# Optimization experiments

Measured on AMD Instinct MI355X. Metric: run time of the kernel, lower is better.

The kernel has to match this reference:

```python
import jax, jax.numpy as jnp
import numpy as np

WS = (8, 8, 8)        # window size
SS = (4, 4, 4)        # shift size
HEADS = 4
DIM = 128
N = WS[0] * WS[1] * WS[2]  # 512 tokens per window


def _relative_position_index():
    # identical math to ShiftedWindowAttention.define_relative_position_index
    coords = np.stack(np.meshgrid(np.arange(WS[0]), np.arange(WS[1]), np.arange(WS[2]), indexing='ij'))
    cf = coords.reshape(3, -1)                       # [3, N]
    rel = (cf[:, :, None] - cf[:, None, :]).transpose(1, 2, 0).copy()  # [N, N, 3]
    rel[..., 0] += WS[0] - 1
    rel[..., 1] += WS[1] - 1
    rel[..., 2] += WS[2] - 1
    rel[..., 0] *= (2 * WS[2] - 1) * (2 * WS[1] - 1)
    rel[..., 1] *= 2 * WS[2] - 1
    return rel.sum(-1).reshape(-1).astype(np.int32)  # [N*N]


def _shift_attn_mask(H, W, D):
    # static shift mask, same as the torch slice-loop construction
    m = np.zeros((H, W, D), dtype=np.float32)
    hs = ((0, -WS[0]), (-WS[0], -SS[0]), (-SS[0], None))
    ws = ((0, -WS[1]), (-WS[1], -SS[1]), (-SS[1], None))
    ds = ((0, -WS[2]), (-WS[2], -SS[2]), (-SS[2], None))
    cnt = 0
    for h in hs:
        for w in ws:
            for d in ds:
                m[h[0]:h[1], w[0]:w[1], d[0]:d[1]] = cnt
                cnt += 1
    nH, nW, nD = H // WS[0], W // WS[1], D // WS[2]
    m = m.reshape(nH, WS[0], nW, WS[1], nD, WS[2]).transpose(0, 2, 4, 1, 3, 5).reshape(nH * nW * nD, N)
    diff = m[:, None, :] - m[:, :, None]
    return np.where(diff != 0, np.float32(-100.0), np.float32(0.0))  # [nWin, N, N]


def setup_inputs() -> dict:
    key = jax.random.key(0)
    ks = jax.random.split(key, 6)
    x = jax.random.normal(ks[0], (1, 32, 32, 32, DIM), dtype=jnp.float32)
    qkv_weight = jax.random.normal(ks[1], (3 * DIM, DIM), dtype=jnp.float32) * 0.02
    qkv_bias = jax.random.normal(ks[2], (3 * DIM,), dtype=jnp.float32) * 0.02
    proj_weight = jax.random.normal(ks[3], (DIM, DIM), dtype=jnp.float32) * 0.02
    proj_bias = jax.random.normal(ks[4], (DIM,), dtype=jnp.float32) * 0.02
    tbl = (2 * WS[0] - 1) * (2 * WS[1] - 1) * (2 * WS[2] - 1)
    rpb_table = jax.random.normal(ks[5], (tbl, HEADS), dtype=jnp.float32) * 0.02
    rp_index = jnp.asarray(_relative_position_index())
    return {"x": x, "qkv_weight": qkv_weight, "qkv_bias": qkv_bias,
            "proj_weight": proj_weight, "proj_bias": proj_bias,
            "rpb_table": rpb_table, "rp_index": rp_index}


def reference(x, qkv_weight, qkv_bias, proj_weight, proj_bias, rpb_table, rp_index):
    B, H, W, D, C = x.shape
    hd = C // HEADS
    # relative position bias: [1, heads, N, N]
    bias = rpb_table[rp_index].reshape(N, N, HEADS).transpose(2, 0, 1)[None]
    # cyclic shift (H,W,D divisible by window -> no padding branch)
    xs = jnp.roll(x, shift=(-SS[0], -SS[1], -SS[2]), axis=(1, 2, 3))
    nH, nW, nD = H // WS[0], W // WS[1], D // WS[2]
    nWin = nH * nW * nD
    # window partition -> [B*nWin, N, C]
    xw = xs.reshape(B, nH, WS[0], nW, WS[1], nD, WS[2], C)
    xw = xw.transpose(0, 1, 3, 5, 2, 4, 6, 7).reshape(B * nWin, N, C)
    qkv = xw @ qkv_weight.T + qkv_bias
    qkv = qkv.reshape(B * nWin, N, 3, HEADS, hd).transpose(2, 0, 3, 1, 4)
    q, k, v = qkv[0], qkv[1], qkv[2]          # each [B*nWin, heads, N, hd]
    q = q * jnp.float32(hd ** -0.5)
    attn = jnp.einsum('whnd,whmd->whnm', q, k) + bias
    mask = jnp.asarray(_shift_attn_mask(H, W, D))  # [nWin, N, N] static
    attn = attn.reshape(B, nWin, HEADS, N, N) + mask[None, :, None]
    attn = jax.nn.softmax(attn.reshape(B * nWin, HEADS, N, N), axis=-1)
    out = jnp.einsum('whnm,whmd->wnhd', attn, v).reshape(B * nWin, N, C)
    out = out @ proj_weight.T + proj_bias
    # reverse window partition
    out = out.reshape(B, nH, nW, nD, WS[0], WS[1], WS[2], C)
    out = out.transpose(0, 1, 4, 2, 5, 3, 6, 7).reshape(B, H, W, D, C)
    return jnp.roll(out, shift=(SS[0], SS[1], SS[2]), axis=(1, 2, 3))
```

## Files before the change

kernel.cpp:

```cpp
#include <hip/hip_runtime.h>
#include <hip/hip_bf16.h>
#include <math.h>


#define NTOT 262144

typedef float     f32x16 __attribute__((ext_vector_type(16)));
typedef __bf16    bf16x8 __attribute__((ext_vector_type(8)));
typedef _Float16  f16x8  __attribute__((ext_vector_type(8)));
typedef _Float16  f16x4  __attribute__((ext_vector_type(4)));
typedef unsigned int u32x4 __attribute__((ext_vector_type(4)));

__device__ __forceinline__ unsigned int pkbf16(float a, float b) {
  __hip_bfloat16 x = __float2bfloat16(a), y = __float2bfloat16(b);
  return (unsigned int)__builtin_bit_cast(unsigned short, x) |
         ((unsigned int)__builtin_bit_cast(unsigned short, y) << 16);
}
__device__ __forceinline__ unsigned short bfbits(float v) {
  return __builtin_bit_cast(unsigned short, __float2bfloat16(v));
}

__global__ void k_bias(const float* __restrict__ rpb, const int* __restrict__ rpi,
                       unsigned short* __restrict__ biasb,
                       const float* __restrict__ qkvw, const float* __restrict__ projw,
                       _Float16* __restrict__ wq, _Float16* __restrict__ wp) {
  int idx = blockIdx.x * 256 + threadIdx.x;
  int t = rpi[idx];
  float4 b4 = *reinterpret_cast<const float4*>(rpb + 4 * t);
  const float L2E = 1.4426950408889634f;
  biasb[0 * NTOT + idx] = bfbits(b4.x * L2E);
  biasb[1 * NTOT + idx] = bfbits(b4.y * L2E);
  biasb[2 * NTOT + idx] = bfbits(b4.z * L2E);
  biasb[3 * NTOT + idx] = bfbits(b4.w * L2E);
  if (idx < 65536) {
    if (idx < 49152) wq[idx] = (_Float16)qkvw[idx];
    else             wp[idx - 49152] = (_Float16)projw[idx - 49152];
  }
}

__global__ __launch_bounds__(256, 2) void k_qkv(
    const float* __restrict__ x, const _Float16* __restrict__ wq,
    const float* __restrict__ qkvb,
    __hip_bfloat16* __restrict__ qb, __hip_bfloat16* __restrict__ kb,
    __hip_bfloat16* __restrict__ vb) {
  __shared__ unsigned short As[128 * 128];
  __shared__ unsigned short Bs[128 * 128];
  const int tid = threadIdx.x;
  const int bm = blockIdx.x;
  const int nc = bm >> 8;
  const int mt = bm & 255;
  const int win = mt >> 2, t128 = mt & 3;
  const int wh = win >> 4, ww = (win >> 2) & 3, wd = win & 3;

#pragma unroll
  for (int u = 0; u < 8; ++u) {
    int f = u * 256 + tid;
    int row = f >> 4, seg = f & 15;
    int n = t128 * 128 + row;
    int lh = n >> 6, lw = (n >> 3) & 7, ld = n & 7;
    int sh = (wh * 8 + lh + 4) & 31;
    int sw = (ww * 8 + lw + 4) & 31;
    int sd = (wd * 8 + ld + 4) & 31;
    const float* src = x + ((sh * 32 + sw) * 32 + sd) * 128 + seg * 8;
    float4 a0 = *(const float4*)src;
    float4 a1 = *(const float4*)(src + 4);
    f16x8 hv;
    hv[0] = (_Float16)a0.x; hv[1] = (_Float16)a0.y;
    hv[2] = (_Float16)a0.z; hv[3] = (_Float16)a0.w;
    hv[4] = (_Float16)a1.x; hv[5] = (_Float16)a1.y;
    hv[6] = (_Float16)a1.z; hv[7] = (_Float16)a1.w;
    int slot = seg ^ (row & 15);
    *(u32x4*)(&As[row * 128 + slot * 8]) = __builtin_bit_cast(u32x4, hv);
  }
#pragma unroll
  for (int u = 0; u < 8; ++u) {
    int f = u * 256 + tid;
    int row = f >> 4, seg = f & 15;
    u32x4 wv = *(const u32x4*)(wq + (nc * 128 + row) * 128 + seg * 8);
    int slot = seg ^ (row & 15);
    *(u32x4*)(&Bs[row * 128 + slot * 8]) = wv;
  }
  __syncthreads();

  const int wave = tid >> 6, lane = tid & 63;
  const int lq = lane & 31, h = lane >> 5;
  const int wm = wave >> 1, wn = wave & 1;

  f32x16 a00, a01, a10, a11;
#pragma unroll
  for (int r = 0; r < 16; ++r) { a00[r] = 0.f; a01[r] = 0.f; a10[r] = 0.f; a11[r] = 0.f; }

#pragma unroll
  for (int ks = 0; ks < 8; ++ks) {
    int r0 = wm * 64 + lq, r1 = wm * 64 + 32 + lq;
    int c0 = wn * 64 + lq, c1 = wn * 64 + 32 + lq;
    int sl = ks * 2 + h;
    f16x8 af0 = __builtin_bit_cast(f16x8, *(const u32x4*)(&As[r0 * 128 + (sl ^ (r0 & 15)) * 8]));
    f16x8 af1 = __builtin_bit_cast(f16x8, *(const u32x4*)(&As[r1 * 128 + (sl ^ (r1 & 15)) * 8]));
    f16x8 bf0 = __builtin_bit_cast(f16x8, *(const u32x4*)(&Bs[c0 * 128 + (sl ^ (c0 & 15)) * 8]));
    f16x8 bf1 = __builtin_bit_cast(f16x8, *(const u32x4*)(&Bs[c1 * 128 + (sl ^ (c1 & 15)) * 8]));
    a00 = __builtin_amdgcn_mfma_f32_32x32x16_f16(af0, bf0, a00, 0, 0, 0);
    a01 = __builtin_amdgcn_mfma_f32_32x32x16_f16(af0, bf1, a01, 0, 0, 0);
    a10 = __builtin_amdgcn_mfma_f32_32x32x16_f16(af1, bf0, a10, 0, 0, 0);
    a11 = __builtin_amdgcn_mfma_f32_32x32x16_f16(af1, bf1, a11, 0, 0, 0);
  }

  const float scale = (float)(0.17677669529663687 * 1.4426950408889634);
  float bias0 = qkvb[nc * 128 + wn * 64 + lq];
  float bias1 = qkvb[nc * 128 + wn * 64 + 32 + lq];

#define EPI_QK(ACC, MI, NI, DST, DO_SCALE)                                    \
  {                                                                           \
    int head = wn * 2 + (NI);                                                 \
    size_t whb = (size_t)(win * 4 + head);                                    \
    float bc = (NI) ? bias1 : bias0;                                          \
    _Pragma("unroll")                                                         \
    for (int r = 0; r < 16; ++r) {                                            \
      int row32 = (r & 3) + 8 * (r >> 2) + 4 * h;                             \
      int n = t128 * 128 + wm * 64 + (MI) * 32 + row32;                       \
      float val = ACC[r] + bc;                                                \
      if (DO_SCALE) val *= scale;                                             \
      DST[(whb * 512 + n) * 32 + lq] = __float2bfloat16(val);                 \
    }                                                                         \
  }
#define EPI_V(ACC, MI, NI)                                                    \
  {                                                                           \
    int head = wn * 2 + (NI);                                                 \
    size_t whb = (size_t)(win * 4 + head);                                    \
    float bc = (NI) ? bias1 : bias0;                                          \
    _Pragma("unroll")                                                         \
    for (int g = 0; g < 4; ++g) {                                             \
      int n0 = t128 * 128 + wm * 64 + (MI) * 32 + g * 8 + 4 * h;              \
      uint2 u = make_uint2(pkbf16(ACC[g * 4 + 0] + bc, ACC[g * 4 + 1] + bc),  \
                           pkbf16(ACC[g * 4 + 2] + bc, ACC[g * 4 + 3] + bc)); \
      *(uint2*)(vb + (whb * 32 + lq) * 512 + n0) = u;                         \
    }                                                                         \
  }

  if (nc == 0) {
    EPI_QK(a00, 0, 0, qb, 1); EPI_QK(a01, 0, 1, qb, 1);
    EPI_QK(a10, 1, 0, qb, 1); EPI_QK(a11, 1, 1, qb, 1);
  } else if (nc == 1) {
    EPI_QK(a00, 0, 0, kb, 0); EPI_QK(a01, 0, 1, kb, 0);
    EPI_QK(a10, 1, 0, kb, 0); EPI_QK(a11, 1, 1, kb, 0);
  } else {
    EPI_V(a00, 0, 0); EPI_V(a01, 0, 1);
    EPI_V(a10, 1, 0); EPI_V(a11, 1, 1);
  }
}

__global__ __launch_bounds__(256) void k_attn(
    const __hip_bfloat16* __restrict__ qb, const __hip_bfloat16* __restrict__ kb,
    const __hip_bfloat16* __restrict__ vb, const unsigned short* __restrict__ biasb,
    _Float16* __restrict__ ao) {
  __shared__ unsigned short Ks[2][64 * 40];
  __shared__ unsigned short Vs[2][32 * 72];
  __shared__ unsigned char regid[512];

  const int tid = threadIdx.x;
  const int b = blockIdx.x;
  const int win = b >> 3, head = (b >> 1) & 3, half = b & 1;
  const int wh = win >> 4, ww = (win >> 2) & 3, wd = win & 3;
  const int wave = tid >> 6, lane = tid & 63;
  const int lq = lane & 31, h = lane >> 5;
  const int qA = half * 256 + wave * 64 + lq;
  const int qB = qA + 32;
  const bool has_mask = (wh == 3) || (ww == 3) || (wd == 3);

  unsigned rnA = 0, rnB = 0;
  if (has_mask) {
#pragma unroll
    for (int i = 0; i < 2; ++i) {
      int n = tid + i * 256;
      int lh = n >> 6, lw = (n >> 3) & 7, ld = n & 7;
      regid[n] = (unsigned char)(((wh == 3) ? (lh < 4 ? 1 : 2) : 0) * 9 +
                                 ((ww == 3) ? (lw < 4 ? 1 : 2) : 0) * 3 +
                                 ((wd == 3) ? (ld < 4 ? 1 : 2) : 0));
    }
    {
      int n = qA;
      int lh = n >> 6, lw = (n >> 3) & 7, ld = n & 7;
      rnA = (unsigned)(((wh == 3) ? (lh < 4 ? 1 : 2) : 0) * 9 +
                       ((ww == 3) ? (lw < 4 ? 1 : 2) : 0) * 3 +
                       ((wd == 3) ? (ld < 4 ? 1 : 2) : 0));
      n = qB; lh = n >> 6; lw = (n >> 3) & 7; ld = n & 7;
      rnB = (unsigned)(((wh == 3) ? (lh < 4 ? 1 : 2) : 0) * 9 +
                       ((ww == 3) ? (lw < 4 ? 1 : 2) : 0) * 3 +
                       ((wd == 3) ? (ld < 4 ? 1 : 2) : 0));
    }
  }

  const size_t whb = (size_t)(win * 4 + head);
  const __hip_bfloat16* qrowA = qb + (whb * 512 + qA) * 32;
  const __hip_bfloat16* qrowB = qb + (whb * 512 + qB) * 32;
  bf16x8 qfA0 = __builtin_bit_cast(bf16x8, *(const u32x4*)(qrowA + h * 8));
  bf16x8 qfA1 = __builtin_bit_cast(bf16x8, *(const u32x4*)(qrowA + 16 + h * 8));
  bf16x8 qfB0 = __builtin_bit_cast(bf16x8, *(const u32x4*)(qrowB + h * 8));
  bf16x8 qfB1 = __builtin_bit_cast(bf16x8, *(const u32x4*)(qrowB + 16 + h * 8));

  const __hip_bfloat16* kg = kb + whb * 512 * 32;
  const __hip_bfloat16* vg = vb + whb * 32 * 512;
  const unsigned short* browA = biasb + ((size_t)head * 512 + qA) * 512;
  const unsigned short* browB = biasb + ((size_t)head * 512 + qB) * 512;

  float lA = 0.f, lB = 0.f;
  f32x16 oA, oB;
#pragma unroll
  for (int r = 0; r < 16; ++r) { oA[r] = 0.f; oB[r] = 0.f; }

  const int srow = tid >> 2, sseg = tid & 3;
  const int svd = tid >> 3, sseg2 = tid & 7;
  u32x4 kreg, vreg;
#define GLOAD(CHK)                                                            \
  { kreg = *(const u32x4*)(kg + ((CHK) * 64 + srow) * 32 + sseg * 8);         \
    vreg = *(const u32x4*)(vg + svd * 512 + (CHK) * 64 + sseg2 * 8); }
#define LWRITE(BUF)                                                           \
  { *(u32x4*)(&Ks[BUF][srow * 40 + sseg * 8]) = kreg;                         \
    *(u32x4*)(&Vs[BUF][svd * 72 + sseg2 * 8]) = vreg; }

  GLOAD(0); LWRITE(0);
  __syncthreads();

  auto stream_step = [&](f32x16 c, const uint2* bb, unsigned rn,
                         float& l_run, f32x16& o,
                         bf16x8 vf0, bf16x8 vf1, int kbase) {
    float p[16];
#pragma unroll
    for (int j = 0; j < 4; ++j) {
      float b0 = __uint_as_float(bb[j].x << 16);
      float b1 = __uint_as_float(bb[j].x & 0xFFFF0000u);
      float b2 = __uint_as_float(bb[j].y << 16);
      float b3 = __uint_as_float(bb[j].y & 0xFFFF0000u);
      if (has_mask) {
        unsigned rm = *(const unsigned*)(&regid[kbase + h * 4 + j * 8]);
        b0 += ((rm & 255u) == rn) ? 0.f : -144.2695041f;
        b1 += (((rm >> 8) & 255u) == rn) ? 0.f : -144.2695041f;
        b2 += (((rm >> 16) & 255u) == rn) ? 0.f : -144.2695041f;
        b3 += (((rm >> 24)) == rn) ? 0.f : -144.2695041f;
      }
      p[j * 4 + 0] = exp2f(c[j * 4 + 0] + b0);
      p[j * 4 + 1] = exp2f(c[j * 4 + 1] + b1);
      p[j * 4 + 2] = exp2f(c[j * 4 + 2] + b2);
      p[j * 4 + 3] = exp2f(c[j * 4 + 3] + b3);
    }
    float s0 = (p[0] + p[1]) + (p[2] + p[3]);
    float s1 = (p[4] + p[5]) + (p[6] + p[7]);
    float s2 = (p[8] + p[9]) + (p[10] + p[11]);
    float s3 = (p[12] + p[13]) + (p[14] + p[15]);
    l_run += (s0 + s1) + (s2 + s3);
    unsigned bw[8];
#pragma unroll
    for (int g = 0; g < 8; ++g) bw[g] = pkbf16(p[2 * g], p[2 * g + 1]);
#pragma unroll
    for (int kc = 0; kc < 2; ++kc) {
      unsigned b0 = bw[kc * 4 + 0], b1 = bw[kc * 4 + 1];
      unsigned b2 = bw[kc * 4 + 2], b3 = bw[kc * 4 + 3];
      unsigned sb0 = __shfl_xor(b0, 32, 64), sb1 = __shfl_xor(b1, 32, 64);
      unsigned sb2 = __shfl_xor(b2, 32, 64), sb3 = __shfl_xor(b3, 32, 64);
      u32x4 pw;
      pw.x = h ? sb2 : b0;
      pw.y = h ? sb3 : b1;
      pw.z = h ? b2 : sb0;
      pw.w = h ? b3 : sb1;
      bf16x8 pf = __builtin_bit_cast(bf16x8, pw);
      o = __builtin_amdgcn_mfma_f32_32x32x16_bf16(kc ? vf1 : vf0, pf, o, 0, 0, 0);
    }
  };

  for (int chk = 0; chk < 8; ++chk) {
    const int cur = chk & 1;
    if (chk < 7) GLOAD(chk + 1);

#pragma unroll
    for (int sub = 0; sub < 2; ++sub) {
      const int kbase = chk * 64 + sub * 32;
      uint2 bbA[4], bbB[4];
#pragma unroll
      for (int j = 0; j < 4; ++j) {
        bbA[j] = *(const uint2*)(browA + kbase + h * 4 + j * 8);
        bbB[j] = *(const uint2*)(browB + kbase + h * 4 + j * 8);
      }
      const unsigned short* KsC = Ks[cur];
      const unsigned short* VsC = Vs[cur];
      bf16x8 kf0 = __builtin_bit_cast(bf16x8, *(const u32x4*)(&KsC[(sub * 32 + lq) * 40 + h * 8]));
      bf16x8 kf1 = __builtin_bit_cast(bf16x8, *(const u32x4*)(&KsC[(sub * 32 + lq) * 40 + 16 + h * 8]));
      f32x16 cA, cB;
#pragma unroll
      for (int r = 0; r < 16; ++r) { cA[r] = 0.f; cB[r] = 0.f; }
      cA = __builtin_amdgcn_mfma_f32_32x32x16_bf16(kf0, qfA0, cA, 0, 0, 0);
      cA = __builtin_amdgcn_mfma_f32_32x32x16_bf16(kf1, qfA1, cA, 0, 0, 0);
      cB = __builtin_amdgcn_mfma_f32_32x32x16_bf16(kf0, qfB0, cB, 0, 0, 0);
      cB = __builtin_amdgcn_mfma_f32_32x32x16_bf16(kf1, qfB1, cB, 0, 0, 0);
      bf16x8 vf0 = __builtin_bit_cast(bf16x8, *(const u32x4*)(&VsC[lq * 72 + sub * 32 + h * 8]));
      bf16x8 vf1 = __builtin_bit_cast(bf16x8, *(const u32x4*)(&VsC[lq * 72 + sub * 32 + 16 + h * 8]));
      stream_step(cA, bbA, rnA, lA, oA, vf0, vf1, kbase);
      stream_step(cB, bbB, rnB, lB, oB, vf0, vf1, kbase);
    }

    if (chk < 7) LWRITE(cur ^ 1);
    __syncthreads();
  }

  lA += __shfl_xor(lA, 32, 64);
  lB += __shfl_xor(lB, 32, 64);

  const float invA = 1.f / lA, invB = 1.f / lB;
  _Float16* orowA = ao + ((size_t)(win * 512 + qA)) * 128 + head * 32;
  _Float16* orowB = ao + ((size_t)(win * 512 + qB)) * 128 + head * 32;
#pragma unroll
  for (int j = 0; j < 4; ++j) {
    int d0 = j * 8 + h * 4;
    f16x4 tA, tB;
    tA[0] = (_Float16)(oA[j * 4 + 0] * invA); tA[1] = (_Float16)(oA[j * 4 + 1] * invA);
    tA[2] = (_Float16)(oA[j * 4 + 2] * invA); tA[3] = (_Float16)(oA[j * 4 + 3] * invA);
    tB[0] = (_Float16)(oB[j * 4 + 0] * invB); tB[1] = (_Float16)(oB[j * 4 + 1] * invB);
    tB[2] = (_Float16)(oB[j * 4 + 2] * invB); tB[3] = (_Float16)(oB[j * 4 + 3] * invB);
    *(f16x4*)(orowA + d0) = tA;
    *(f16x4*)(orowB + d0) = tB;
  }
}

__global__ __launch_bounds__(256, 2) void k_proj(
    const _Float16* __restrict__ ao, const _Float16* __restrict__ wp,
    const float* __restrict__ pb, float* __restrict__ out) {
  __shared__ unsigned short As[128 * 128];
  __shared__ unsigned short Bs[128 * 128];
  const int tid = threadIdx.x;
  const int mt = blockIdx.x;
  const int win = mt >> 2, t128 = mt & 3;
  const int wh = win >> 4, ww = (win >> 2) & 3, wd = win & 3;

#pragma unroll
  for (int u = 0; u < 8; ++u) {
    int f = u * 256 + tid;
    int row = f >> 4, seg = f & 15;
    u32x4 av = *(const u32x4*)(ao + ((size_t)(win * 512 + t128 * 128 + row)) * 128 + seg * 8);
    int slot = seg ^ (row & 15);
    *(u32x4*)(&As[row * 128 + slot * 8]) = av;
  }
#pragma unroll
  for (int u = 0; u < 8; ++u) {
    int f = u * 256 + tid;
    int row = f >> 4, seg = f & 15;
    u32x4 wv = *(const u32x4*)(wp + row * 128 + seg * 8);
    int slot = seg ^ (row & 15);
    *(u32x4*)(&Bs[row * 128 + slot * 8]) = wv;
  }
  __syncthreads();

  const int wave = tid >> 6, lane = tid & 63;
  const int lq = lane & 31, h = lane >> 5;
  const int wm = wave >> 1, wn = wave & 1;

  f32x16 a00, a01, a10, a11;
#pragma unroll
  for (int r = 0; r < 16; ++r) { a00[r] = 0.f; a01[r] = 0.f; a10[r] = 0.f; a11[r] = 0.f; }

#pragma unroll
  for (int ks = 0; ks < 8; ++ks) {
    int r0 = wm * 64 + lq, r1 = wm * 64 + 32 + lq;
    int c0 = wn * 64 + lq, c1 = wn * 64 + 32 + lq;
    int sl = ks * 2 + h;
    f16x8 af0 = __builtin_bit_cast(f16x8, *(const u32x4*)(&As[r0 * 128 + (sl ^ (r0 & 15)) * 8]));
    f16x8 af1 = __builtin_bit_cast(f16x8, *(const u32x4*)(&As[r1 * 128 + (sl ^ (r1 & 15)) * 8]));
    f16x8 bf0 = __builtin_bit_cast(f16x8, *(const u32x4*)(&Bs[c0 * 128 + (sl ^ (c0 & 15)) * 8]));
    f16x8 bf1 = __builtin_bit_cast(f16x8, *(const u32x4*)(&Bs[c1 * 128 + (sl ^ (c1 & 15)) * 8]));
    a00 = __builtin_amdgcn_mfma_f32_32x32x16_f16(af0, bf0, a00, 0, 0, 0);
    a01 = __builtin_amdgcn_mfma_f32_32x32x16_f16(af0, bf1, a01, 0, 0, 0);
    a10 = __builtin_amdgcn_mfma_f32_32x32x16_f16(af1, bf0, a10, 0, 0, 0);
    a11 = __builtin_amdgcn_mfma_f32_32x32x16_f16(af1, bf1, a11, 0, 0, 0);
  }

  float bias0 = pb[wn * 64 + lq];
  float bias1 = pb[wn * 64 + 32 + lq];

#define EPI_P(ACC, MI, NI)                                                    \
  {                                                                           \
    int col = wn * 64 + (NI) * 32 + lq;                                       \
    float bc = (NI) ? bias1 : bias0;                                          \
    _Pragma("unroll")                                                         \
    for (int r = 0; r < 16; ++r) {                                            \
      int row32 = (r & 3) + 8 * (r >> 2) + 4 * h;                             \
      int n = t128 * 128 + wm * 64 + (MI) * 32 + row32;                       \
      int lh = n >> 6, lw = (n >> 3) & 7, ld = n & 7;                         \
      int dh = (wh * 8 + lh + 4) & 31;                                        \
      int dw = (ww * 8 + lw + 4) & 31;                                        \
      int dd = (wd * 8 + ld + 4) & 31;                                        \
      out[(size_t)((dh * 32 + dw) * 32 + dd) * 128 + col] = ACC[r] + bc;      \
    }                                                                         \
  }
  EPI_P(a00, 0, 0); EPI_P(a01, 0, 1); EPI_P(a10, 1, 0); EPI_P(a11, 1, 1);
}

extern "C" void kernel_launch(void* const* d_in, const int* in_sizes, int n_in,
                              void* d_out, int out_size, void* d_ws, size_t ws_size,
                              hipStream_t stream) {
  const float* x    = (const float*)d_in[0];
  const float* qkvw = (const float*)d_in[1];
  const float* qkvb = (const float*)d_in[2];
  const float* pw   = (const float*)d_in[3];
  const float* pb   = (const float*)d_in[4];
  const float* rpb  = (const float*)d_in[5];
  const int*   rpi  = (const int*)d_in[6];
  float* out = (float*)d_out;

  char* base = (char*)d_ws;
  __hip_bfloat16* qbuf = (__hip_bfloat16*)(base);
  __hip_bfloat16* kbuf = (__hip_bfloat16*)(base + 8388608);
  __hip_bfloat16* vbuf = (__hip_bfloat16*)(base + 16777216);
  _Float16* ao = (_Float16*)(base + 25165824);
  unsigned short* biasb = (unsigned short*)(base + 33554432);
  _Float16* wq = (_Float16*)(base + 35651584);
  _Float16* wp = (_Float16*)(base + 35749888);

  hipLaunchKernelGGL(k_bias, dim3(1024), dim3(256), 0, stream, rpb, rpi, biasb, qkvw, pw, wq, wp);
  hipLaunchKernelGGL(k_qkv,  dim3(768),  dim3(256), 0, stream, x, wq, qkvb, qbuf, kbuf, vbuf);
  hipLaunchKernelGGL(k_attn, dim3(512),  dim3(256), 0, stream, qbuf, kbuf, vbuf, biasb, ao);
  hipLaunchKernelGGL(k_proj, dim3(256),  dim3(256), 0, stream, ao, wp, pb, out);
}
```

Measured before the change: 155.6 us.

## Split attention blocks to one query tile per wave, doubling grid and occupancy

Each wave now handles 32 query rows instead of 64, so the attention grid doubles to 1024 blocks, and launch bounds request 4 blocks per CU. This cuts accumulator register pressure and raises occupancy to better hide latency. Bias loads for both sub-chunks are hoisted ahead of the K/V prefetch, and V fragments are loaded per MFMA. The cost is that every K/V chunk is loaded into LDS twice as many times, since each block now reuses it across fewer queries.

```diff
diff --git a/kernel.cpp b/kernel.cpp
--- a/kernel.cpp
+++ b/kernel.cpp
@@ -149,7 +149,7 @@
   }
 }
 
-__global__ __launch_bounds__(256) void k_attn(
+__global__ __launch_bounds__(256, 4) void k_attn(
     const __hip_bfloat16* __restrict__ qb, const __hip_bfloat16* __restrict__ kb,
     const __hip_bfloat16* __restrict__ vb, const unsigned short* __restrict__ biasb,
     _Float16* __restrict__ ao) {
@@ -159,15 +159,14 @@
 
   const int tid = threadIdx.x;
   const int b = blockIdx.x;
-  const int win = b >> 3, head = (b >> 1) & 3, half = b & 1;
+  const int win = b >> 4, head = (b >> 2) & 3, qblk = b & 3;
   const int wh = win >> 4, ww = (win >> 2) & 3, wd = win & 3;
   const int wave = tid >> 6, lane = tid & 63;
   const int lq = lane & 31, h = lane >> 5;
-  const int qA = half * 256 + wave * 64 + lq;
-  const int qB = qA + 32;
+  const int q = qblk * 128 + wave * 32 + lq;
   const bool has_mask = (wh == 3) || (ww == 3) || (wd == 3);
 
-  unsigned rnA = 0, rnB = 0;
+  unsigned rn = 0;
   if (has_mask) {
 #pragma unroll
     for (int i = 0; i < 2; ++i) {
@@ -177,36 +176,25 @@
                                  ((ww == 3) ? (lw < 4 ? 1 : 2) : 0) * 3 +
                                  ((wd == 3) ? (ld < 4 ? 1 : 2) : 0));
     }
-    {
-      int n = qA;
-      int lh = n >> 6, lw = (n >> 3) & 7, ld = n & 7;
-      rnA = (unsigned)(((wh == 3) ? (lh < 4 ? 1 : 2) : 0) * 9 +
-                       ((ww == 3) ? (lw < 4 ? 1 : 2) : 0) * 3 +
-                       ((wd == 3) ? (ld < 4 ? 1 : 2) : 0));
-      n = qB; lh = n >> 6; lw = (n >> 3) & 7; ld = n & 7;
-      rnB = (unsigned)(((wh == 3) ? (lh < 4 ? 1 : 2) : 0) * 9 +
-                       ((ww == 3) ? (lw < 4 ? 1 : 2) : 0) * 3 +
-                       ((wd == 3) ? (ld < 4 ? 1 : 2) : 0));
-    }
+    int lh = q >> 6, lw = (q >> 3) & 7, ld = q & 7;
+    rn = (unsigned)(((wh == 3) ? (lh < 4 ? 1 : 2) : 0) * 9 +
+                    ((ww == 3) ? (lw < 4 ? 1 : 2) : 0) * 3 +
+                    ((wd == 3) ? (ld < 4 ? 1 : 2) : 0));
   }
 
   const size_t whb = (size_t)(win * 4 + head);
-  const __hip_bfloat16* qrowA = qb + (whb * 512 + qA) * 32;
-  const __hip_bfloat16* qrowB = qb + (whb * 512 + qB) * 32;
-  bf16x8 qfA0 = __builtin_bit_cast(bf16x8, *(const u32x4*)(qrowA + h * 8));
-  bf16x8 qfA1 = __builtin_bit_cast(bf16x8, *(const u32x4*)(qrowA + 16 + h * 8));
-  bf16x8 qfB0 = __builtin_bit_cast(bf16x8, *(const u32x4*)(qrowB + h * 8));
-  bf16x8 qfB1 = __builtin_bit_cast(bf16x8, *(const u32x4*)(qrowB + 16 + h * 8));
+  const __hip_bfloat16* qrow = qb + (whb * 512 + q) * 32;
+  bf16x8 qf0 = __builtin_bit_cast(bf16x8, *(const u32x4*)(qrow + h * 8));
+  bf16x8 qf1 = __builtin_bit_cast(bf16x8, *(const u32x4*)(qrow + 16 + h * 8));
 
   const __hip_bfloat16* kg = kb + whb * 512 * 32;
   const __hip_bfloat16* vg = vb + whb * 32 * 512;
-  const unsigned short* browA = biasb + ((size_t)head * 512 + qA) * 512;
-  const unsigned short* browB = biasb + ((size_t)head * 512 + qB) * 512;
-
-  float lA = 0.f, lB = 0.f;
-  f32x16 oA, oB;
-#pragma unroll
-  for (int r = 0; r < 16; ++r) { oA[r] = 0.f; oB[r] = 0.f; }
+  const unsigned short* brow = biasb + ((size_t)head * 512 + q) * 512;
+
+  float l_run = 0.f;
+  f32x16 o;
+#pragma unroll
+  for (int r = 0; r < 16; ++r) o[r] = 0.f;
 
   const int srow = tid >> 2, sseg = tid & 3;
   const int svd = tid >> 3, sseg2 = tid & 7;
@@ -221,102 +209,94 @@
   GLOAD(0); LWRITE(0);
   __syncthreads();
 
-  auto stream_step = [&](f32x16 c, const uint2* bb, unsigned rn,
-                         float& l_run, f32x16& o,
-                         bf16x8 vf0, bf16x8 vf1, int kbase) {
-    float p[16];
-#pragma unroll
-    for (int j = 0; j < 4; ++j) {
-      float b0 = __uint_as_float(bb[j].x << 16);
-      float b1 = __uint_as_float(bb[j].x & 0xFFFF0000u);
-      float b2 = __uint_as_float(bb[j].y << 16);
-      float b3 = __uint_as_float(bb[j].y & 0xFFFF0000u);
-      if (has_mask) {
-        unsigned rm = *(const unsigned*)(&regid[kbase + h * 4 + j * 8]);
-        b0 += ((rm & 255u) == rn) ? 0.f : -144.2695041f;
-        b1 += (((rm >> 8) & 255u) == rn) ? 0.f : -144.2695041f;
-        b2 += (((rm >> 16) & 255u) == rn) ? 0.f : -144.2695041f;
-        b3 += (((rm >> 24)) == rn) ? 0.f : -144.2695041f;
-      }
-      p[j * 4 + 0] = exp2f(c[j * 4 + 0] + b0);
-      p[j * 4 + 1] = exp2f(c[j * 4 + 1] + b1);
-      p[j * 4 + 2] = exp2f(c[j * 4 + 2] + b2);
-      p[j * 4 + 3] = exp2f(c[j * 4 + 3] + b3);
-    }
-    float s0 = (p[0] + p[1]) + (p[2] + p[3]);
-    float s1 = (p[4] + p[5]) + (p[6] + p[7]);
-    float s2 = (p[8] + p[9]) + (p[10] + p[11]);
-    float s3 = (p[12] + p[13]) + (p[14] + p[15]);
-    l_run += (s0 + s1) + (s2 + s3);
-    unsigned bw[8];
-#pragma unroll
-    for (int g = 0; g < 8; ++g) bw[g] = pkbf16(p[2 * g], p[2 * g + 1]);
-#pragma unroll
-    for (int kc = 0; kc < 2; ++kc) {
-      unsigned b0 = bw[kc * 4 + 0], b1 = bw[kc * 4 + 1];
-      unsigned b2 = bw[kc * 4 + 2], b3 = bw[kc * 4 + 3];
-      unsigned sb0 = __shfl_xor(b0, 32, 64), sb1 = __shfl_xor(b1, 32, 64);
-      unsigned sb2 = __shfl_xor(b2, 32, 64), sb3 = __shfl_xor(b3, 32, 64);
-      u32x4 pw;
-      pw.x = h ? sb2 : b0;
-      pw.y = h ? sb3 : b1;
-      pw.z = h ? b2 : sb0;
-      pw.w = h ? b3 : sb1;
-      bf16x8 pf = __builtin_bit_cast(bf16x8, pw);
-      o = __builtin_amdgcn_mfma_f32_32x32x16_bf16(kc ? vf1 : vf0, pf, o, 0, 0, 0);
-    }
-  };
-
   for (int chk = 0; chk < 8; ++chk) {
     const int cur = chk & 1;
+
+    uint2 bb[2][4];
+#pragma unroll
+    for (int sub = 0; sub < 2; ++sub)
+#pragma unroll
+      for (int j = 0; j < 4; ++j)
+        bb[sub][j] = *(const uint2*)(brow + chk * 64 + sub * 32 + h * 4 + j * 8);
+
     if (chk < 7) GLOAD(chk + 1);
 
 #pragma unroll
     for (int sub = 0; sub < 2; ++sub) {
       const int kbase = chk * 64 + sub * 32;
-      uint2 bbA[4], bbB[4];
-#pragma unroll
-      for (int j = 0; j < 4; ++j) {
-        bbA[j] = *(const uint2*)(browA + kbase + h * 4 + j * 8);
-        bbB[j] = *(const uint2*)(browB + kbase + h * 4 + j * 8);
-      }
       const unsigned short* KsC = Ks[cur];
       const unsigned short* VsC = Vs[cur];
       bf16x8 kf0 = __builtin_bit_cast(bf16x8, *(const u32x4*)(&KsC[(sub * 32 + lq) * 40 + h * 8]));
       bf16x8 kf1 = __builtin_bit_cast(bf16x8, *(const u32x4*)(&KsC[(sub * 32 + lq) * 40 + 16 + h * 8]));
-      f32x16 cA, cB;
-#pragma unroll
-      for (int r = 0; r < 16; ++r) { cA[r] = 0.f; cB[r] = 0.f; }
-      cA = __builtin_amdgcn_mfma_f32_32x32x16_bf16(kf0, qfA0, cA, 0, 0, 0);
-      cA = __builtin_amdgcn_mfma_f32_32x32x16_bf16(kf1, qfA1, cA, 0, 0, 0);
-      cB = __builtin_amdgcn_mfma_f32_32x32x16_bf16(kf0, qfB0, cB, 0, 0, 0);
-      cB = __builtin_amdgcn_mfma_f32_32x32x16_bf16(kf1, qfB1, cB, 0, 0, 0);
-      bf16x8 vf0 = __builtin_bit_cast(bf16x8, *(const u32x4*)(&VsC[lq * 72 + sub * 32 + h * 8]));
-      bf16x8 vf1 = __builtin_bit_cast(bf16x8, *(const u32x4*)(&VsC[lq * 72 + sub * 32 + 16 + h * 8]));
-      stream_step(cA, bbA, rnA, lA, oA, vf0, vf1, kbase);
-      stream_step(cB, bbB, rnB, lB, oB, vf0, vf1, kbase);
+      f32x16 c;
+#pragma unroll
+      for (int r = 0; r < 16; ++r) c[r] = 0.f;
+      c = __builtin_amdgcn_mfma_f32_32x32x16_bf16(kf0, qf0, c, 0, 0, 0);
+      c = __builtin_amdgcn_mfma_f32_32x32x16_bf16(kf1, qf1, c, 0, 0, 0);
+
+      float p[16];
+#pragma unroll
+      for (int j = 0; j < 4; ++j) {
+        float b0 = __uint_as_float(bb[sub][j].x << 16);
+        float b1 = __uint_as_float(bb[sub][j].x & 0xFFFF0000u);
+        float b2 = __uint_as_float(bb[sub][j].y << 16);
+        float b3 = __uint_as_float(bb[sub][j].y & 0xFFFF0000u);
+        if (has_mask) {
+          unsigned rm = *(const unsigned*)(&regid[kbase + h * 4 + j * 8]);
+          b0 += ((rm & 255u) == rn) ? 0.f : -144.2695041f;
+          b1 += (((rm >> 8) & 255u) == rn) ? 0.f : -144.2695041f;
+          b2 += (((rm >> 16) & 255u) == rn) ? 0.f : -144.2695041f;
+          b3 += (((rm >> 24)) == rn) ? 0.f : -144.2695041f;
+        }
+        p[j * 4 + 0] = exp2f(c[j * 4 + 0] + b0);
+        p[j * 4 + 1] = exp2f(c[j * 4 + 1] + b1);
+        p[j * 4 + 2] = exp2f(c[j * 4 + 2] + b2);
+        p[j * 4 + 3] = exp2f(c[j * 4 + 3] + b3);
+      }
+      float s0 = (p[0] + p[1]) + (p[2] + p[3]);
+      float s1 = (p[4] + p[5]) + (p[6] + p[7]);
+      float s2 = (p[8] + p[9]) + (p[10] + p[11]);
+      float s3 = (p[12] + p[13]) + (p[14] + p[15]);
+      l_run += (s0 + s1) + (s2 + s3);
+
+      unsigned bw[8];
+#pragma unroll
+      for (int g = 0; g < 8; ++g) bw[g] = pkbf16(p[2 * g], p[2 * g + 1]);
+#pragma unroll
+      for (int kc = 0; kc < 2; ++kc) {
+        unsigned b0 = bw[kc * 4 + 0], b1 = bw[kc * 4 + 1];
+        unsigned b2 = bw[kc * 4 + 2], b3 = bw[kc * 4 + 3];
+        unsigned sb0 = __shfl_xor(b0, 32, 64), sb1 = __shfl_xor(b1, 32, 64);
+        unsigned sb2 = __shfl_xor(b2, 32, 64), sb3 = __shfl_xor(b3, 32, 64);
+        u32x4 pw;
+        pw.x = h ? sb2 : b0;
+        pw.y = h ? sb3 : b1;
+        pw.z = h ? b2 : sb0;
+        pw.w = h ? b3 : sb1;
+        bf16x8 pf = __builtin_bit_cast(bf16x8, pw);
+        bf16x8 vf = __builtin_bit_cast(bf16x8,
+            *(const u32x4*)(&VsC[lq * 72 + sub * 32 + kc * 16 + h * 8]));
+        o = __builtin_amdgcn_mfma_f32_32x32x16_bf16(vf, pf, o, 0, 0, 0);
+      }
     }
 
     if (chk < 7) LWRITE(cur ^ 1);
     __syncthreads();
   }
 
-  lA += __shfl_xor(lA, 32, 64);
-  lB += __shfl_xor(lB, 32, 64);
-
-  const float invA = 1.f / lA, invB = 1.f / lB;
-  _Float16* orowA = ao + ((size_t)(win * 512 + qA)) * 128 + head * 32;
-  _Float16* orowB = ao + ((size_t)(win * 512 + qB)) * 128 + head * 32;
+  l_run += __shfl_xor(l_run, 32, 64);
+
+  const float inv = 1.f / l_run;
+  _Float16* orow = ao + ((size_t)(win * 512 + q)) * 128 + head * 32;
 #pragma unroll
   for (int j = 0; j < 4; ++j) {
     int d0 = j * 8 + h * 4;
-    f16x4 tA, tB;
-    tA[0] = (_Float16)(oA[j * 4 + 0] * invA); tA[1] = (_Float16)(oA[j * 4 + 1] * invA);
-    tA[2] = (_Float16)(oA[j * 4 + 2] * invA); tA[3] = (_Float16)(oA[j * 4 + 3] * invA);
-    tB[0] = (_Float16)(oB[j * 4 + 0] * invB); tB[1] = (_Float16)(oB[j * 4 + 1] * invB);
-    tB[2] = (_Float16)(oB[j * 4 + 2] * invB); tB[3] = (_Float16)(oB[j * 4 + 3] * invB);
-    *(f16x4*)(orowA + d0) = tA;
-    *(f16x4*)(orowB + d0) = tB;
+    f16x4 t;
+    t[0] = (_Float16)(o[j * 4 + 0] * inv);
+    t[1] = (_Float16)(o[j * 4 + 1] * inv);
+    t[2] = (_Float16)(o[j * 4 + 2] * inv);
+    t[3] = (_Float16)(o[j * 4 + 3] * inv);
+    *(f16x4*)(orow + d0) = t;
   }
 }
 
@@ -415,6 +395,6 @@
 
   hipLaunchKernelGGL(k_bias, dim3(1024), dim3(256), 0, stream, rpb, rpi, biasb, qkvw, pw, wq, wp);
   hipLaunchKernelGGL(k_qkv,  dim3(768),  dim3(256), 0, stream, x, wq, qkvb, qbuf, kbuf, vbuf);
-  hipLaunchKernelGGL(k_attn, dim3(512),  dim3(256), 0, stream, qbuf, kbuf, vbuf, biasb, ao);
+  hipLaunchKernelGGL(k_attn, dim3(1024), dim3(256), 0, stream, qbuf, kbuf, vbuf, biasb, ao);
   hipLaunchKernelGGL(k_proj, dim3(256),  dim3(256), 0, stream, ao, wp, pb, out);
 }
```

After: 144.4 us. 7.2% less time.
